# Performance work log

Measured on AMD Instinct MI355X. Metric: run time of the kernel, lower is better.

The kernel has to match this reference:

```python
import jax, jax.numpy as jnp
import numpy as np
import math

B, S, D, H = 8, 1024, 1024, 16
HD = D // H  # head_features = 64
SCALE = math.sqrt(HD)


def setup_inputs() -> dict:
    key = jax.random.key(0)
    k0, k1, k2, k3, k4 = jax.random.split(key, 5)
    x = jax.random.normal(k0, (B, S, D), dtype=jnp.float32)
    attn_mask = (jax.random.uniform(k1, (B, S, S)) < 0.9).astype(jnp.float32)
    w_scale = 1.0 / math.sqrt(D)  # keep unsafe exp in finite range
    Wq = jax.random.normal(k2, (D, D), dtype=jnp.float32) * w_scale
    Wk = jax.random.normal(k3, (D, D), dtype=jnp.float32) * w_scale
    Wv = jax.random.normal(k4, (D, D), dtype=jnp.float32) * w_scale
    return {"x": x, "attn_mask": attn_mask, "Wq": Wq, "Wk": Wk, "Wv": Wv}


def reference(x, attn_mask, Wq, Wk, Wv):
    b, s, _ = x.shape

    def split_heads(t):  # [b,s,D] -> [b,H,s,HD]
        return t.reshape(b, s, H, HD).transpose(0, 2, 1, 3)

    q = split_heads(x @ Wq)
    k = split_heads(x @ Wk)
    v = split_heads(x @ Wv)

    # unsafe softmax: exp without max subtraction, multiplicative mask, +1e-8 denom
    scores = jnp.einsum('bhsd,bhtd->bhst', q, k) / SCALE
    e = jnp.exp(scores) * attn_mask[:, None, :, :]
    w = e / (e.sum(axis=3, keepdims=True) + 1e-8)

    ctx = jnp.einsum('bhst,bhtd->bhsd', w, v)  # [b,H,s,HD]
    return ctx.transpose(0, 2, 1, 3).reshape(b, s, D)
```

## Files before the change

### kernel.cpp

```cpp
#include <hip/hip_runtime.h>

#define KDIM 1024

typedef _Float16 half8 __attribute__((ext_vector_type(8)));
typedef _Float16 half4 __attribute__((ext_vector_type(4)));
typedef __fp16 fp16x2 __attribute__((ext_vector_type(2)));
typedef __fp16 fp16x4 __attribute__((ext_vector_type(4)));
typedef float f32x4 __attribute__((ext_vector_type(4)));

#if defined(__has_builtin)
#if __has_builtin(__builtin_amdgcn_global_load_lds)
#define HAVE_GLDS 1
#endif
#if __has_builtin(__builtin_amdgcn_exp2f)
#define EXP2(x) __builtin_amdgcn_exp2f(x)
#endif
#if __has_builtin(__builtin_amdgcn_cvt_pkrtz)
#define HAVE_PKRTZ 1
#endif
#if __has_builtin(__builtin_amdgcn_fdot2)
#define HAVE_FDOT2 1
#endif
#endif
#ifndef EXP2
#define EXP2(x) exp2f(x)
#endif

__device__ __forceinline__ void stage16(const _Float16* g, _Float16* wave_base, int lane) {
#ifdef HAVE_GLDS
  __builtin_amdgcn_global_load_lds(
      (const __attribute__((address_space(1))) void*)g,
      (__attribute__((address_space(3))) void*)wave_base, 16, 0, 0);
#else
  *(half8*)(wave_base + lane * 8) = *(const half8*)g;
#endif
}

#define BARRIER() __builtin_amdgcn_s_barrier()
#define LGKM0()                                         \
  do {                                                  \
    asm volatile("s_waitcnt lgkmcnt(0)" ::: "memory");  \
    __builtin_amdgcn_sched_barrier(0);                  \
  } while (0)
#define VMCNT(n)                                               \
  do {                                                         \
    asm volatile("s_waitcnt vmcnt(" #n ")" ::: "memory");      \
  } while (0)

__global__ void prep_kernel(const float* __restrict__ x, const float* __restrict__ am,
                            const float* __restrict__ Wq, const float* __restrict__ Wk,
                            const float* __restrict__ Wv, _Float16* __restrict__ xb,
                            _Float16* __restrict__ Wqkvt, unsigned long long* __restrict__ bits) {
  __shared__ _Float16 tile[32][33];
  int bid = blockIdx.x;
  if (bid < 8192) {
    size_t i = ((size_t)bid * 256 + threadIdx.x) * 4;
    float4 v = *(const float4*)(x + i);
    half4 h = { (_Float16)v.x, (_Float16)v.y, (_Float16)v.z, (_Float16)v.w };
    *(half4*)(xb + i) = h;
  } else if (bid < 11264) {
    int zz = bid - 8192;
    int z = zz >> 10;
    int rem = zz & 1023;
    int bx = rem & 31, by = rem >> 5;
    const float* src = z == 0 ? Wq : (z == 1 ? Wk : Wv);
    _Float16* dst = Wqkvt + (size_t)z * KDIM * KDIM;
    float sc = (z == 0) ? 0.18033688011112042f : 1.0f;
    int tx = threadIdx.x & 31, ty = threadIdx.x >> 5;
    int c0 = bx * 32, r0 = by * 32;
#pragma unroll
    for (int i = 0; i < 4; i++) {
      int r = r0 + ty + i * 8;
      tile[tx][ty + i * 8] = (_Float16)(src[(size_t)r * KDIM + c0 + tx] * sc);
    }
    __syncthreads();
#pragma unroll
    for (int i = 0; i < 4; i++) {
      int n = c0 + ty + i * 8;
      dst[(size_t)n * KDIM + r0 + tx] = tile[ty + i * 8][tx];
    }
  } else {
    size_t i = (size_t)(bid - 11264) * 256 + threadIdx.x;
    unsigned long long b = __ballot(am[i] != 0.0f);
    if ((threadIdx.x & 63) == 0) bits[i >> 6] = b;
  }
}

__global__ __launch_bounds__(512, 2)
void gemm_kernel(const _Float16* __restrict__ A, const _Float16* __restrict__ Bt,
                 _Float16* __restrict__ Qt, _Float16* __restrict__ Kh,
                 _Float16* __restrict__ Vth) {
  __shared__ _Float16 As[2 * 16384];
  __shared__ _Float16 Bs[2 * 12288];
  int tid = threadIdx.x;
  int lane = tid & 63, w = tid >> 6;
  int la = lane & 15, qd = lane >> 4;
  int wm = w & 1, wn = w >> 1;
  int bid = blockIdx.x;
  int wg = (bid & 7) * 64 + (bid >> 3);
  int by = wg >> 4, bx = wg & 15;
  int m0 = by * 256, n0 = bx * 192;
  int srow = tid >> 3;
  int scc = ((srow & 7) ^ (tid & 7)) << 3;
  const int rc0 = ((qd ^ (la & 7)) << 3);
  const int rc1 = (((4 | qd) ^ (la & 7)) << 3);

  const _Float16* Ab = A + (size_t)m0 * KDIM;
  const _Float16* Bb = Bt + (size_t)n0 * KDIM;

  const _Float16* pA0a = Ab + (size_t)(srow) * KDIM + scc;
  const _Float16* pA0b = Ab + (size_t)(srow + 64) * KDIM + scc;
  const _Float16* pA1a = Ab + (size_t)(srow + 128) * KDIM + scc;
  const _Float16* pA1b = Ab + (size_t)(srow + 192) * KDIM + scc;
  const _Float16* pB0 = Bb + (size_t)(srow) * KDIM + scc;
  const _Float16* pB1 = Bb + (size_t)(srow + 64) * KDIM + scc;
  const _Float16* pB2 = Bb + (size_t)(srow + 128) * KDIM + scc;

  _Float16* ldsAw = As + w * 512;
  _Float16* ldsBw = Bs + w * 512;

  const _Float16* baseA0 = As + wm * 4096 + la * 64 + rc0;
  const _Float16* baseA1 = As + wm * 4096 + la * 64 + rc1;
  const _Float16* baseB0 = Bs + (wn * 16 + la) * 64 + rc0;
  const _Float16* baseB1 = Bs + (wn * 16 + la) * 64 + rc1;

  f32x4 acc[8][3] = {};
  half8 af[4][2], bf0[2], bf1[2], bf2[2];

#define STAGE_A0(B)                                       \
  do {                                                    \
    stage16(pA0a, ldsAw + (B) * 16384, lane);             \
    stage16(pA0b, ldsAw + (B) * 16384 + 4096, lane);      \
    pA0a += 64; pA0b += 64;                               \
  } while (0)
#define STAGE_A1(B)                                       \
  do {                                                    \
    stage16(pA1a, ldsAw + (B) * 16384 + 8192, lane);      \
    stage16(pA1b, ldsAw + (B) * 16384 + 12288, lane);     \
    pA1a += 64; pA1b += 64;                               \
  } while (0)
#define STAGE_B0(B)                                       \
  do { stage16(pB0, ldsBw + (B) * 12288, lane); pB0 += 64; } while (0)
#define STAGE_B1(B)                                       \
  do { stage16(pB1, ldsBw + (B) * 12288 + 4096, lane); pB1 += 64; } while (0)
#define STAGE_B2(B)                                       \
  do { stage16(pB2, ldsBw + (B) * 12288 + 8192, lane); pB2 += 64; } while (0)
#define LD_AF(CUR, MH)                                                               \
  do {                                                                               \
    _Pragma("unroll") for (int mi = 0; mi < 4; ++mi) {                               \
      af[mi][0] = *(const half8*)(baseA0 + (CUR) * 16384 + (MH) * 8192 + mi * 1024); \
      af[mi][1] = *(const half8*)(baseA1 + (CUR) * 16384 + (MH) * 8192 + mi * 1024); \
    }                                                                                \
  } while (0)
#define LD_B(BF, CUR, NJ)                                                  \
  do {                                                                     \
    BF[0] = *(const half8*)(baseB0 + (CUR) * 12288 + (NJ) * 4096);         \
    BF[1] = *(const half8*)(baseB1 + (CUR) * 12288 + (NJ) * 4096);         \
  } while (0)
#define MFMA_N(MH, NJ, BF)                                                          \
  do {                                                                              \
    _Pragma("unroll") for (int mi = 0; mi < 4; ++mi) {                              \
      acc[(MH) * 4 + mi][NJ] = __builtin_amdgcn_mfma_f32_16x16x32_f16(              \
          af[mi][0], BF[0], acc[(MH) * 4 + mi][NJ], 0, 0, 0);                       \
      acc[(MH) * 4 + mi][NJ] = __builtin_amdgcn_mfma_f32_16x16x32_f16(              \
          af[mi][1], BF[1], acc[(MH) * 4 + mi][NJ], 0, 0, 0);                       \
    }                                                                               \
  } while (0)

  STAGE_A0(0); STAGE_B0(0); STAGE_A1(0); STAGE_B1(0); STAGE_B2(0);
  VMCNT(0);
  BARRIER();

#define KTILE(T, CUR, NXT)                                     \
  do {                                                         \
    int t = (T);                                               \
                                                  \
    LD_AF(CUR, 0);                                             \
    LD_B(bf0, CUR, 0);                                         \
    if (t < 15) { STAGE_A0(NXT); STAGE_B0(NXT); }              \
    BARRIER();                                                 \
    LGKM0();                                                   \
    __builtin_amdgcn_s_setprio(1);                             \
    MFMA_N(0, 0, bf0);                                         \
    __builtin_amdgcn_s_setprio(0);                             \
    if (t < 15) { VMCNT(3); } else { VMCNT(0); }               \
    BARRIER();                                                 \
                                                  \
    LD_B(bf1, CUR, 1);                                         \
    LD_B(bf2, CUR, 2);                                         \
    if (t < 15) STAGE_A1(NXT);                                 \
    BARRIER();                                                 \
    LGKM0();                                                   \
    __builtin_amdgcn_s_setprio(1);                             \
    MFMA_N(0, 1, bf1);                                         \
    MFMA_N(0, 2, bf2);                                         \
    __builtin_amdgcn_s_setprio(0);                             \
    BARRIER();                                                 \
                                                  \
    LD_AF(CUR, 1);                                             \
    if (t < 15) { STAGE_B1(NXT); STAGE_B2(NXT); }              \
    BARRIER();                                                 \
    LGKM0();                                                   \
    __builtin_amdgcn_s_setprio(1);                             \
    MFMA_N(1, 0, bf0);                                         \
    MFMA_N(1, 1, bf1);                                         \
    MFMA_N(1, 2, bf2);                                         \
    __builtin_amdgcn_s_setprio(0);                             \
    if (t < 15) { VMCNT(4); }                                  \
    BARRIER();                                                 \
  } while (0)

#pragma unroll 1
  for (int tp = 0; tp < 8; ++tp) {
    KTILE(2 * tp, 0, 1);
    KTILE(2 * tp + 1, 1, 0);
  }

#undef KTILE
#undef MFMA_N
#undef LD_B
#undef LD_AF
#undef STAGE_B2
#undef STAGE_B1
#undef STAGE_B0
#undef STAGE_A1
#undef STAGE_A0

  int rr = lane >> 2, c4 = lane & 3;
  _Float16* ep = As + w * 1280;
#pragma unroll
  for (int mh = 0; mh < 2; ++mh) {
    int srow0 = m0 + mh * 128 + wm * 64;
    int b = srow0 >> 10, s0 = srow0 & 1023;
#pragma unroll
    for (int nj = 0; nj < 3; ++nj) {
      int colh = n0 + wn * 16 + nj * 64;
      int whichf = colh >> 10;
      int cm = colh & 1023;
      int hh = cm >> 6, d0 = cm & 63;
      if (whichf == 1) {
        _Float16* kb = Kh + (size_t)(b * 16 + hh) * 1024 * 64;
#pragma unroll
        for (int mi = 0; mi < 4; ++mi) {
          f32x4 v = acc[mh * 4 + mi][nj];
          int s = s0 + mi * 16 + qd * 4;
#pragma unroll
          for (int rg = 0; rg < 4; ++rg)
            kb[(size_t)(s + rg) * 64 + d0 + la] = (_Float16)v[rg];
        }
      } else {
        _Float16* dst = (whichf == 0) ? Qt : Vth;
#pragma unroll
        for (int mi = 0; mi < 4; ++mi) {
          f32x4 v = acc[mh * 4 + mi][nj];
          half4 hv = { (_Float16)v[0], (_Float16)v[1], (_Float16)v[2], (_Float16)v[3] };
          *(half4*)(ep + la * 72 + mi * 16 + qd * 4) = hv;
        }
        half8 o0 = *(const half8*)(ep + rr * 72 + c4 * 16);
        half8 o1 = *(const half8*)(ep + rr * 72 + c4 * 16 + 8);
        _Float16* gp = dst + ((size_t)(b * 16 + hh) * 64 + d0 + rr) * 1024 + s0 + c4 * 16;
        *(half8*)gp = o0;
        *(half8*)(gp + 8) = o1;
      }
    }
  }
}

__global__ __launch_bounds__(512, 2)
void attn_kernel(const _Float16* __restrict__ Qt, const _Float16* __restrict__ K,
                 const _Float16* __restrict__ Vt, const unsigned long long* __restrict__ mbits,
                 float* __restrict__ out) {
  __shared__ _Float16 Ks[4][2 * 64 * 32];
  __shared__ _Float16 Vs[2][2 * 64 * 40];
  int tid = threadIdx.x;
  int lane = tid & 63, w4 = tid >> 6;
  int la = lane & 15, qd = lane >> 4;
  int linear = blockIdx.x;
  int xlo = linear & 7;
  int tmp = linear >> 3;
  int qt = tmp & 3;
  int hb = (tmp >> 2) * 8 + xlo;
  int h = hb & 15, b = hb >> 4;
  const _Float16* Qp = Qt + (size_t)hb * 64 * 1024;
  const _Float16* Kp = K + (size_t)hb * 1024 * 64;
  const _Float16* Vp = Vt + (size_t)hb * 64 * 1024;
  int q0w = qt * 256 + w4 * 16;
  half8 qf[2][2];
#pragma unroll
  for (int qi = 0; qi < 2; qi++)
#pragma unroll
    for (int ks = 0; ks < 2; ks++)
#pragma unroll
      for (int j = 0; j < 8; j++)
        qf[qi][ks][j] = Qp[(size_t)(ks * 32 + qd * 8 + j) * 1024 + q0w + qi * 128 + la];
  unsigned long long mq[2][4];
#pragma unroll
  for (int qi = 0; qi < 2; qi++) {
    const ulonglong2* mp =
        (const ulonglong2*)(mbits + ((size_t)b * 1024 + q0w + qi * 128 + la) * 16 + qd * 4);
    ulonglong2 m01 = mp[0];
    ulonglong2 m23 = mp[1];
    mq[qi][0] = m01.x; mq[qi][1] = m01.y; mq[qi][2] = m23.x; mq[qi][3] = m23.y;
  }
  f32x4 acco[2][4] = {};
  float rs[2] = {0.f, 0.f};
  int kt_t = (tid & 255) >> 2;
  int kt_d = (tid >> 8) * 32 + (((tid & 3) ^ ((tid >> 2) & 3) ^ ((tid >> 4) & 3)) << 3);
  int kc8 = ((qd ^ (la & 3) ^ (la >> 2)) << 3);
  int vd = tid >> 3;
  int vt = (tid & 7) * 8;
  int vs_off = (vt >= 32 ? 2560 : 0) + vd * 40 + (vt & 31);
#if defined(HAVE_FDOT2) && defined(HAVE_PKRTZ)
  fp16x2 one2 = { (__fp16)1.0f, (__fp16)1.0f };
#endif
  {
    half8 vv0 = *(const half8*)(Vp + (size_t)vd * 1024 + vt);
    __builtin_amdgcn_sched_barrier(0);
    stage16(Kp + (size_t)kt_t * 64 + kt_d, Ks[0] + w4 * 512, lane);
    stage16(Kp + (size_t)(64 + kt_t) * 64 + kt_d, Ks[1] + w4 * 512, lane);
    *(half8*)(Vs[0] + vs_off) = vv0;
  }
  asm volatile("s_waitcnt vmcnt(1) lgkmcnt(0)" ::: "memory");
  BARRIER();
  for (int tt = 0; tt < 16; tt++) {
    const _Float16* ks_ = Ks[tt & 3];
    const _Float16* vs_ = Vs[tt & 1];
    half8 vvn;
    if (tt < 15) {
      vvn = *(const half8*)(Vp + (size_t)vd * 1024 + (tt + 1) * 64 + vt);
      __builtin_amdgcn_sched_barrier(0);
    }
    if (tt < 14)
      stage16(Kp + (size_t)((tt + 2) * 64 + kt_t) * 64 + kt_d, Ks[(tt + 2) & 3] + w4 * 512, lane);
    unsigned long long mw0 = __shfl(mq[0][tt & 3], ((tt >> 2) << 4) + la);
    unsigned long long mw1 = __shfl(mq[1][tt & 3], ((tt >> 2) << 4) + la);
    unsigned long long mq0s = mw0 >> (qd * 4);
    unsigned long long mq1s = mw1 >> (qd * 4);
#pragma unroll
    for (int tsub = 0; tsub < 4; tsub++) {
      half8 kf0 = *(const half8*)(ks_ + (tsub * 16 + la) * 32 + kc8);
      half8 kf1 = *(const half8*)(ks_ + 2048 + (tsub * 16 + la) * 32 + kc8);
      f32x4 a0 = {}, a1 = {};
      __builtin_amdgcn_s_setprio(1);
      a0 = __builtin_amdgcn_mfma_f32_16x16x32_f16(kf0, qf[0][0], a0, 0, 0, 0);
      a1 = __builtin_amdgcn_mfma_f32_16x16x32_f16(kf0, qf[1][0], a1, 0, 0, 0);
      a0 = __builtin_amdgcn_mfma_f32_16x16x32_f16(kf1, qf[0][1], a0, 0, 0, 0);
      a1 = __builtin_amdgcn_mfma_f32_16x16x32_f16(kf1, qf[1][1], a1, 0, 0, 0);
      __builtin_amdgcn_s_setprio(0);
      half4 pf[2];
#pragma unroll
      for (int qi = 0; qi < 2; qi++) {
        const f32x4& aa = qi ? a1 : a0;
        unsigned nib = (unsigned)((qi ? mq1s : mq0s) >> (tsub * 16)) & 15u;
        float e0 = (nib & 1u) ? EXP2(aa[0]) : 0.0f;
        float e1 = (nib & 2u) ? EXP2(aa[1]) : 0.0f;
        float e2 = (nib & 4u) ? EXP2(aa[2]) : 0.0f;
        float e3 = (nib & 8u) ? EXP2(aa[3]) : 0.0f;
#ifdef HAVE_PKRTZ
        fp16x2 p01 = __builtin_amdgcn_cvt_pkrtz(e0, e1);
        fp16x2 p23 = __builtin_amdgcn_cvt_pkrtz(e2, e3);
        fp16x4 pfv = __builtin_shufflevector(p01, p23, 0, 1, 2, 3);
        pf[qi] = __builtin_bit_cast(half4, pfv);
#else
        pf[qi][0] = (_Float16)e0; pf[qi][1] = (_Float16)e1;
        pf[qi][2] = (_Float16)e2; pf[qi][3] = (_Float16)e3;
#endif
#if defined(HAVE_FDOT2) && defined(HAVE_PKRTZ)
        rs[qi] = __builtin_amdgcn_fdot2(p01, one2, rs[qi], false);
        rs[qi] = __builtin_amdgcn_fdot2(p23, one2, rs[qi], false);
#else
        rs[qi] += e0 + e1 + e2 + e3;
#endif
      }
#pragma unroll
      for (int nsub = 0; nsub < 4; nsub++) {
        half4 vf = *(const half4*)(vs_ + (tsub >> 1) * 2560 + (nsub * 16 + la) * 40 +
                                   (tsub & 1) * 16 + qd * 4);
        __builtin_amdgcn_s_setprio(1);
        acco[0][nsub] = __builtin_amdgcn_mfma_f32_16x16x16f16(pf[0], vf, acco[0][nsub], 0, 0, 0);
        acco[1][nsub] = __builtin_amdgcn_mfma_f32_16x16x16f16(pf[1], vf, acco[1][nsub], 0, 0, 0);
        __builtin_amdgcn_s_setprio(0);
      }
    }
    if (tt < 15) *(half8*)(Vs[(tt + 1) & 1] + vs_off) = vvn;
    if (tt < 14) {
      asm volatile("s_waitcnt vmcnt(1) lgkmcnt(0)" ::: "memory");
      BARRIER();
    } else if (tt == 14) {
      asm volatile("s_waitcnt vmcnt(0) lgkmcnt(0)" ::: "memory");
      BARRIER();
    }
  }
  float* op = out + (size_t)b * 1024 * 1024 + (size_t)h * 64;
#pragma unroll
  for (int qi = 0; qi < 2; qi++) {
    float r0 = rs[qi];
    r0 += __shfl_xor(r0, 16);
    r0 += __shfl_xor(r0, 32);
    float inv_q = 1.0f / (r0 + 1e-8f);
#pragma unroll
    for (int rg = 0; rg < 4; rg++) {
      float inv = __shfl(inv_q, qd * 4 + rg);
      int s = q0w + qi * 128 + qd * 4 + rg;
#pragma unroll
      for (int nsub = 0; nsub < 4; nsub++)
        op[(size_t)s * 1024 + nsub * 16 + la] = acco[qi][nsub][rg] * inv;
    }
  }
}

extern "C" void kernel_launch(void* const* d_in, const int* in_sizes, int n_in,
                              void* d_out, int out_size, void* d_ws, size_t ws_size,
                              hipStream_t stream) {
  (void)in_sizes; (void)n_in; (void)out_size; (void)ws_size;
  const float* x = (const float*)d_in[0];
  const float* am = (const float*)d_in[1];
  const float* Wq = (const float*)d_in[2];
  const float* Wk = (const float*)d_in[3];
  const float* Wv = (const float*)d_in[4];
  float* out = (float*)d_out;

  char* p = (char*)d_ws;
  _Float16* xb = (_Float16*)p;    p += (size_t)8192 * 1024 * 2;
  _Float16* Wqkvt = (_Float16*)p; p += (size_t)3 * 1024 * 1024 * 2;
  _Float16* Qt = (_Float16*)p;    p += (size_t)8192 * 1024 * 2;
  _Float16* Kh = (_Float16*)p;    p += (size_t)8192 * 1024 * 2;
  _Float16* Vth = (_Float16*)p;   p += (size_t)8192 * 1024 * 2;
  unsigned long long* mb = (unsigned long long*)p;

  prep_kernel<<<44032, 256, 0, stream>>>(x, am, Wq, Wk, Wv, xb, Wqkvt, mb);
  gemm_kernel<<<dim3(512), 512, 0, stream>>>(xb, Wqkvt, Qt, Kh, Vth);
  attn_kernel<<<512, 512, 0, stream>>>(Qt, Kh, Vth, mb, out);
}
```

Baseline: 247.6 us.

## Simplify QKV GEMM pipeline to K=32 tiles with single sync per tile

```diff
diff --git a/kernel.cpp b/kernel.cpp
--- a/kernel.cpp
+++ b/kernel.cpp
@@ -37,15 +37,6 @@
 }
 
 #define BARRIER() __builtin_amdgcn_s_barrier()
-#define LGKM0()                                         \
-  do {                                                  \
-    asm volatile("s_waitcnt lgkmcnt(0)" ::: "memory");  \
-    __builtin_amdgcn_sched_barrier(0);                  \
-  } while (0)
-#define VMCNT(n)                                               \
-  do {                                                         \
-    asm volatile("s_waitcnt vmcnt(" #n ")" ::: "memory");      \
-  } while (0)
 
 __global__ void prep_kernel(const float* __restrict__ x, const float* __restrict__ am,
                             const float* __restrict__ Wq, const float* __restrict__ Wk,
@@ -86,12 +77,12 @@
   }
 }
 
-__global__ __launch_bounds__(512, 2)
+__global__ __launch_bounds__(512, 4)
 void gemm_kernel(const _Float16* __restrict__ A, const _Float16* __restrict__ Bt,
                  _Float16* __restrict__ Qt, _Float16* __restrict__ Kh,
                  _Float16* __restrict__ Vth) {
-  __shared__ _Float16 As[2 * 16384];
-  __shared__ _Float16 Bs[2 * 12288];
+  __shared__ _Float16 As[2 * 8192];
+  __shared__ _Float16 Bs[2 * 6144];
   int tid = threadIdx.x;
   int lane = tid & 63, w = tid >> 6;
   int la = lane & 15, qd = lane >> 4;
@@ -100,131 +91,65 @@
   int wg = (bid & 7) * 64 + (bid >> 3);
   int by = wg >> 4, bx = wg & 15;
   int m0 = by * 256, n0 = bx * 192;
-  int srow = tid >> 3;
-  int scc = ((srow & 7) ^ (tid & 7)) << 3;
-  const int rc0 = ((qd ^ (la & 7)) << 3);
-  const int rc1 = (((4 | qd) ^ (la & 7)) << 3);
-
+
+  int srow = lane >> 2;
+  int slc = ((lane & 3) ^ ((lane >> 3) & 3)) << 3;
   const _Float16* Ab = A + (size_t)m0 * KDIM;
   const _Float16* Bb = Bt + (size_t)n0 * KDIM;
-
-  const _Float16* pA0a = Ab + (size_t)(srow) * KDIM + scc;
-  const _Float16* pA0b = Ab + (size_t)(srow + 64) * KDIM + scc;
-  const _Float16* pA1a = Ab + (size_t)(srow + 128) * KDIM + scc;
-  const _Float16* pA1b = Ab + (size_t)(srow + 192) * KDIM + scc;
-  const _Float16* pB0 = Bb + (size_t)(srow) * KDIM + scc;
-  const _Float16* pB1 = Bb + (size_t)(srow + 64) * KDIM + scc;
-  const _Float16* pB2 = Bb + (size_t)(srow + 128) * KDIM + scc;
-
-  _Float16* ldsAw = As + w * 512;
-  _Float16* ldsBw = Bs + w * 512;
-
-  const _Float16* baseA0 = As + wm * 4096 + la * 64 + rc0;
-  const _Float16* baseA1 = As + wm * 4096 + la * 64 + rc1;
-  const _Float16* baseB0 = Bs + (wn * 16 + la) * 64 + rc0;
-  const _Float16* baseB1 = Bs + (wn * 16 + la) * 64 + rc1;
+  const _Float16* pAa = Ab + (size_t)(w * 16 + srow) * KDIM + slc;
+  const _Float16* pAb = Ab + (size_t)(128 + w * 16 + srow) * KDIM + slc;
+  const _Float16* pBa = Bb + (size_t)(w * 16 + srow) * KDIM + slc;
+  const _Float16* pBb = Bb + (size_t)(128 + w * 16 + srow) * KDIM + slc;
+
+  _Float16* ldsA0 = As + w * 512;
+  _Float16* ldsA1 = As + 4096 + w * 512;
+  _Float16* ldsB0 = Bs + w * 512;
+  _Float16* ldsB1 = Bs + 4096 + w * 512;
+
+  const int rc = ((qd ^ ((la >> 1) & 3)) << 3);
+  const _Float16* baseA = As + (wm * 64 + la) * 32 + rc;
+  const _Float16* baseB = Bs + (wn * 16 + la) * 32 + rc;
 
   f32x4 acc[8][3] = {};
-  half8 af[4][2], bf0[2], bf1[2], bf2[2];
-
-#define STAGE_A0(B)                                       \
-  do {                                                    \
-    stage16(pA0a, ldsAw + (B) * 16384, lane);             \
-    stage16(pA0b, ldsAw + (B) * 16384 + 4096, lane);      \
-    pA0a += 64; pA0b += 64;                               \
+  half8 bf[3];
+
+#define STAGE_AB(B)                                            \
+  do {                                                         \
+    stage16(pAa, ldsA0 + (B) * 8192, lane);                    \
+    stage16(pAb, ldsA1 + (B) * 8192, lane);                    \
+    stage16(pBa, ldsB0 + (B) * 6144, lane);                    \
+    if (w < 4) stage16(pBb, ldsB1 + (B) * 6144, lane);         \
+    pAa += 32; pAb += 32; pBa += 32; pBb += 32;                \
   } while (0)
-#define STAGE_A1(B)                                       \
-  do {                                                    \
-    stage16(pA1a, ldsAw + (B) * 16384 + 8192, lane);      \
-    stage16(pA1b, ldsAw + (B) * 16384 + 12288, lane);     \
-    pA1a += 64; pA1b += 64;                               \
+
+#define TILE(T, CUR, NXT)                                                       \
+  do {                                                                          \
+    if ((T) < 31) STAGE_AB(NXT);                                                \
+    _Pragma("unroll") for (int nj = 0; nj < 3; ++nj)                            \
+        bf[nj] = *(const half8*)(baseB + (CUR) * 6144 + nj * 2048);             \
+    __builtin_amdgcn_s_setprio(1);                                              \
+    _Pragma("unroll") for (int a = 0; a < 8; ++a) {                             \
+      half8 afa = *(const half8*)(baseA + (CUR) * 8192 + (a >> 2) * 4096 +      \
+                                  (a & 3) * 512);                               \
+      _Pragma("unroll") for (int nj = 0; nj < 3; ++nj)                          \
+          acc[a][nj] = __builtin_amdgcn_mfma_f32_16x16x32_f16(                  \
+              afa, bf[nj], acc[a][nj], 0, 0, 0);                                \
+    }                                                                           \
+    __builtin_amdgcn_s_setprio(0);                                              \
+    __syncthreads();                                                            \
   } while (0)
-#define STAGE_B0(B)                                       \
-  do { stage16(pB0, ldsBw + (B) * 12288, lane); pB0 += 64; } while (0)
-#define STAGE_B1(B)                                       \
-  do { stage16(pB1, ldsBw + (B) * 12288 + 4096, lane); pB1 += 64; } while (0)
-#define STAGE_B2(B)                                       \
-  do { stage16(pB2, ldsBw + (B) * 12288 + 8192, lane); pB2 += 64; } while (0)
-#define LD_AF(CUR, MH)                                                               \
-  do {                                                                               \
-    _Pragma("unroll") for (int mi = 0; mi < 4; ++mi) {                               \
-      af[mi][0] = *(const half8*)(baseA0 + (CUR) * 16384 + (MH) * 8192 + mi * 1024); \
-      af[mi][1] = *(const half8*)(baseA1 + (CUR) * 16384 + (MH) * 8192 + mi * 1024); \
-    }                                                                                \
-  } while (0)
-#define LD_B(BF, CUR, NJ)                                                  \
-  do {                                                                     \
-    BF[0] = *(const half8*)(baseB0 + (CUR) * 12288 + (NJ) * 4096);         \
-    BF[1] = *(const half8*)(baseB1 + (CUR) * 12288 + (NJ) * 4096);         \
-  } while (0)
-#define MFMA_N(MH, NJ, BF)                                                          \
-  do {                                                                              \
-    _Pragma("unroll") for (int mi = 0; mi < 4; ++mi) {                              \
-      acc[(MH) * 4 + mi][NJ] = __builtin_amdgcn_mfma_f32_16x16x32_f16(              \
-          af[mi][0], BF[0], acc[(MH) * 4 + mi][NJ], 0, 0, 0);                       \
-      acc[(MH) * 4 + mi][NJ] = __builtin_amdgcn_mfma_f32_16x16x32_f16(              \
-          af[mi][1], BF[1], acc[(MH) * 4 + mi][NJ], 0, 0, 0);                       \
-    }                                                                               \
-  } while (0)
-
-  STAGE_A0(0); STAGE_B0(0); STAGE_A1(0); STAGE_B1(0); STAGE_B2(0);
-  VMCNT(0);
-  BARRIER();
-
-#define KTILE(T, CUR, NXT)                                     \
-  do {                                                         \
-    int t = (T);                                               \
-                                                  \
-    LD_AF(CUR, 0);                                             \
-    LD_B(bf0, CUR, 0);                                         \
-    if (t < 15) { STAGE_A0(NXT); STAGE_B0(NXT); }              \
-    BARRIER();                                                 \
-    LGKM0();                                                   \
-    __builtin_amdgcn_s_setprio(1);                             \
-    MFMA_N(0, 0, bf0);                                         \
-    __builtin_amdgcn_s_setprio(0);                             \
-    if (t < 15) { VMCNT(3); } else { VMCNT(0); }               \
-    BARRIER();                                                 \
-                                                  \
-    LD_B(bf1, CUR, 1);                                         \
-    LD_B(bf2, CUR, 2);                                         \
-    if (t < 15) STAGE_A1(NXT);                                 \
-    BARRIER();                                                 \
-    LGKM0();                                                   \
-    __builtin_amdgcn_s_setprio(1);                             \
-    MFMA_N(0, 1, bf1);                                         \
-    MFMA_N(0, 2, bf2);                                         \
-    __builtin_amdgcn_s_setprio(0);                             \
-    BARRIER();                                                 \
-                                                  \
-    LD_AF(CUR, 1);                                             \
-    if (t < 15) { STAGE_B1(NXT); STAGE_B2(NXT); }              \
-    BARRIER();                                                 \
-    LGKM0();                                                   \
-    __builtin_amdgcn_s_setprio(1);                             \
-    MFMA_N(1, 0, bf0);                                         \
-    MFMA_N(1, 1, bf1);                                         \
-    MFMA_N(1, 2, bf2);                                         \
-    __builtin_amdgcn_s_setprio(0);                             \
-    if (t < 15) { VMCNT(4); }                                  \
-    BARRIER();                                                 \
-  } while (0)
+
+  STAGE_AB(0);
+  __syncthreads();
 
 #pragma unroll 1
-  for (int tp = 0; tp < 8; ++tp) {
-    KTILE(2 * tp, 0, 1);
-    KTILE(2 * tp + 1, 1, 0);
-  }
-
-#undef KTILE
-#undef MFMA_N
-#undef LD_B
-#undef LD_AF
-#undef STAGE_B2
-#undef STAGE_B1
-#undef STAGE_B0
-#undef STAGE_A1
-#undef STAGE_A0
+  for (int tp = 0; tp < 16; ++tp) {
+    TILE(2 * tp, 0, 1);
+    TILE(2 * tp + 1, 1, 0);
+  }
+
+#undef TILE
+#undef STAGE_AB
 
   int rr = lane >> 2, c4 = lane & 3;
   _Float16* ep = As + w * 1280;
```

After: 240.6 us. -2.8%, faster.
